# Optimization experiments

Measured on AMD Instinct MI355X. Metric: run time of the kernel, lower is better.

The kernel has to match this reference:

```python
import jax, jax.numpy as jnp
import numpy as np

TEMP = 0.1
DX = 64  # feature dim of x; W1 rows [0:DX] multiply x, rows [DX:] multiply y


def setup_inputs() -> dict:
    key = jax.random.key(0)
    k1, k2, k3, k4 = jax.random.split(key, 4)
    n, d, hidden = 1024, 64, 256
    x = jax.random.normal(k1, (n, d), dtype=jnp.float32)
    y = jax.random.normal(k2, (n, d), dtype=jnp.float32)
    W1 = jax.random.normal(k3, (2 * d, hidden), dtype=jnp.float32) * (1.0 / np.sqrt(2 * d))
    b1 = jnp.zeros((hidden,), dtype=jnp.float32)
    w2 = jax.random.normal(k4, (hidden,), dtype=jnp.float32) * (1.0 / np.sqrt(hidden))
    b2 = jnp.zeros((), dtype=jnp.float32)
    return {"x": x, "y": y, "W1": W1, "b1": b1, "w2": w2, "b2": b2}


def reference(x, y, W1, b1, w2, b2):
    n = y.shape[0]
    W1x, W1y = W1[:DX], W1[DX:]
    xp = x @ W1x                      # [n, hidden], indexed by j (x_tile[i,j] = x[j])
    yp = y @ W1y                      # [n, hidden], indexed by i (y_tile[i,j] = y[i])
    # Positive pairs: scorer(cat(x_i, y_i))
    pos = (jax.nn.relu(xp + yp + b1) @ w2 + b2) / TEMP          # [n]
    h = jax.nn.relu(yp[:, None, :] + xp[None, :, :] + b1)        # [n, n, hidden]
    scores = (h @ w2 + b2) / TEMP                                 # [n, n]
    lse = jax.nn.logsumexp(scores, axis=1)                        # [n]
    lower_bound = pos.mean() - (lse.mean() - jnp.log(jnp.float32(n)))
    return -lower_bound
```

## Files before the change

kernel.cpp:

```cpp
#include <hip/hip_runtime.h>
#include <math.h>

#define NN 1024
#define DD 64
#define HH 256
#define TEMP_INV 10.0f

typedef float v2f __attribute__((ext_vector_type(2)));


__global__ __launch_bounds__(256)
void k1_proj(const float* __restrict__ x, const float* __restrict__ y,
             const float* __restrict__ W1, const float* __restrict__ b1,
             float* __restrict__ x2T, float* __restrict__ y2)
{
    const int tid = threadIdx.x;
    const int i0 = blockIdx.x * 2;
    float ax0 = 0.f, ax1 = 0.f, ay0 = 0.f, ay1 = 0.f;
    #pragma unroll 8
    for (int kk = 0; kk < DD; ++kk) {
        const float wx = W1[kk * HH + tid];
        const float wy = W1[(DD + kk) * HH + tid];
        ax0 = fmaf(x[i0 * DD + kk],       wx, ax0);
        ax1 = fmaf(x[(i0 + 1) * DD + kk], wx, ax1);
        ay0 = fmaf(y[i0 * DD + kk],       wy, ay0);
        ay1 = fmaf(y[(i0 + 1) * DD + kk], wy, ay1);
    }
    const float b1t = b1[tid];
    *(float2*)&x2T[tid * NN + i0] = make_float2(ax0 + b1t, ax1 + b1t);
    y2[i0 * HH + tid]       = ay0;
    y2[(i0 + 1) * HH + tid] = ay1;
}

__global__ __launch_bounds__(256)
void k2_scores(const float* __restrict__ x2T, const float* __restrict__ y2,
               const float* __restrict__ w2, const float* __restrict__ b2,
               float* __restrict__ pmax, float* __restrict__ psum,
               float* __restrict__ pos)
{
    const int t  = threadIdx.x;
    const int bj = blockIdx.x;
    const int bi = blockIdx.y;
    const int j0 = bj * 64;
    const int rbase = bi * 32 + (t >> 5) * 4;
    const int cc = t & 31;

    const float* yb = y2 + (size_t)rbase * HH;
    const float* xb = x2T + j0 + cc * 2;

    v2f a0 = {0.f, 0.f}, a1 = {0.f, 0.f}, a2 = {0.f, 0.f}, a3 = {0.f, 0.f};
    const v2f zero = {0.f, 0.f};

    #pragma unroll 2
    for (int g = 0; g < HH / 4; ++g) {
        const int kb = g * 4;
        const float4 yr0 = *(const float4*)&yb[kb];
        const float4 yr1 = *(const float4*)&yb[HH + kb];
        const float4 yr2 = *(const float4*)&yb[2 * HH + kb];
        const float4 yr3 = *(const float4*)&yb[3 * HH + kb];
        const v2f xv0 = *(const v2f*)&xb[(size_t)(kb + 0) * NN];
        const v2f xv1 = *(const v2f*)&xb[(size_t)(kb + 1) * NN];
        const v2f xv2 = *(const v2f*)&xb[(size_t)(kb + 2) * NN];
        const v2f xv3 = *(const v2f*)&xb[(size_t)(kb + 3) * NN];
#define STEP(XV, Y0, Y1, Y2, Y3, WK)                                          \
        {                                                                     \
            const float wk = (WK);                                            \
            const v2f wv = {wk, wk};                                          \
            v2f z;                                                            \
            z = XV + (v2f){(Y0), (Y0)};                                       \
            z = __builtin_elementwise_max(z, zero);                           \
            a0 = z * wv + a0;                                                 \
            z = XV + (v2f){(Y1), (Y1)};                                       \
            z = __builtin_elementwise_max(z, zero);                           \
            a1 = z * wv + a1;                                                 \
            z = XV + (v2f){(Y2), (Y2)};                                       \
            z = __builtin_elementwise_max(z, zero);                           \
            a2 = z * wv + a2;                                                 \
            z = XV + (v2f){(Y3), (Y3)};                                       \
            z = __builtin_elementwise_max(z, zero);                           \
            a3 = z * wv + a3;                                                 \
        }
        STEP(xv0, yr0.x, yr1.x, yr2.x, yr3.x, w2[kb + 0])
        STEP(xv1, yr0.y, yr1.y, yr2.y, yr3.y, w2[kb + 1])
        STEP(xv2, yr0.z, yr1.z, yr2.z, yr3.z, w2[kb + 2])
        STEP(xv3, yr0.w, yr1.w, yr2.w, yr3.w, w2[kb + 3])
#undef STEP
    }

    const float bb = b2[0];
    const v2f bbv = {bb, bb};
    v2f sc[4];
    sc[0] = (a0 + bbv) * TEMP_INV;
    sc[1] = (a1 + bbv) * TEMP_INV;
    sc[2] = (a2 + bbv) * TEMP_INV;
    sc[3] = (a3 + bbv) * TEMP_INV;

    const int col0 = j0 + cc * 2;
    #pragma unroll
    for (int p = 0; p < 4; ++p) {
        const int row = rbase + p;
        if (row == col0)     pos[row] = sc[p].x;
        if (row == col0 + 1) pos[row] = sc[p].y;
    }

    float m[4], e[4];
    #pragma unroll
    for (int p = 0; p < 4; ++p) {
        m[p] = fmaxf(sc[p].x, sc[p].y);
        e[p] = __expf(sc[p].x - m[p]) + __expf(sc[p].y - m[p]);
    }
    #pragma unroll
    for (int mk = 16; mk >= 1; mk >>= 1) {
        #pragma unroll
        for (int p = 0; p < 4; ++p) {
            const float mo = __shfl_xor(m[p], mk);
            const float eo = __shfl_xor(e[p], mk);
            const float mn = fmaxf(m[p], mo);
            e[p] = e[p] * __expf(m[p] - mn) + eo * __expf(mo - mn);
            m[p] = mn;
        }
    }
    if (cc == 0) {
        #pragma unroll
        for (int p = 0; p < 4; ++p) {
            pmax[bj * NN + rbase + p] = m[p];
            psum[bj * NN + rbase + p] = e[p];
        }
    }
}

__global__ __launch_bounds__(1024)
void k3_final(const float* __restrict__ pmax, const float* __restrict__ psum,
              const float* __restrict__ pos, float* __restrict__ out)
{
    __shared__ float2 red[1024];
    const int tid = threadIdx.x;
    float M = pmax[tid], E = psum[tid];
    #pragma unroll
    for (int jc = 1; jc < 16; ++jc) {
        const float Mo = pmax[jc * NN + tid];
        const float Eo = psum[jc * NN + tid];
        const float Mn = fmaxf(M, Mo);
        E = E * __expf(M - Mn) + Eo * __expf(Mo - Mn);
        M = Mn;
    }
    red[tid] = make_float2(M + logf(E), pos[tid]);
    __syncthreads();
    for (int s = 512; s > 0; s >>= 1) {
        if (tid < s) {
            const float2 o = red[tid + s];
            float2 m2 = red[tid];
            m2.x += o.x; m2.y += o.y;
            red[tid] = m2;
        }
        __syncthreads();
    }
    if (tid == 0)
        out[0] = red[0].x / (float)NN - logf((float)NN) - red[0].y / (float)NN;
}

extern "C" void kernel_launch(void* const* d_in, const int* in_sizes, int n_in,
                              void* d_out, int out_size, void* d_ws, size_t ws_size,
                              hipStream_t stream)
{
    const float* x  = (const float*)d_in[0];
    const float* y  = (const float*)d_in[1];
    const float* W1 = (const float*)d_in[2];
    const float* b1 = (const float*)d_in[3];
    const float* w2 = (const float*)d_in[4];
    const float* b2 = (const float*)d_in[5];
    float* out = (float*)d_out;

    float* ws   = (float*)d_ws;
    float* x2T  = ws;
    float* y2   = x2T + HH * NN;
    float* pmax = y2 + NN * HH;
    float* psum = pmax + 16 * NN;
    float* pos  = psum + 16 * NN;

    hipLaunchKernelGGL(k1_proj, dim3(NN / 2), dim3(256), 0, stream,
                       x, y, W1, b1, x2T, y2);
    hipLaunchKernelGGL(k2_scores, dim3(16, 32), dim3(256), 0, stream,
                       x2T, y2, w2, b2, pmax, psum, pos);
    hipLaunchKernelGGL(k3_final, dim3(1), dim3(1024), 0, stream,
                       pmax, psum, pos, out);
}
```

Before: 47.10 us.

## Stage x2T tiles through LDS with register double-buffered prefetch in k2

The scores kernel now copies 64-row chunks of the transposed x projection into shared memory, cooperatively loading with float4, and prefetches the next chunk into registers while computing on the current one. y rows are also software-pipelined one step ahead in registers, and launch bounds request two blocks per CU. The aim is to replace strided per-thread global loads of x2T with coalesced loads and to hide their latency. The cost is extra syncthreads, LDS traffic and register pressure.

Measured after the change: 136.9 us. +190.7%, slower.

```diff
diff --git a/kernel.cpp b/kernel.cpp
--- a/kernel.cpp
+++ b/kernel.cpp
@@ -5,6 +5,8 @@
 #define DD 64
 #define HH 256
 #define TEMP_INV 10.0f
+#define KCH 64
+#define NCH 4
 
 typedef float v2f __attribute__((ext_vector_type(2)));
 
@@ -32,68 +34,85 @@
     y2[(i0 + 1) * HH + tid] = ay1;
 }
 
-__global__ __launch_bounds__(256)
+__global__ __launch_bounds__(256, 2)
 void k2_scores(const float* __restrict__ x2T, const float* __restrict__ y2,
                const float* __restrict__ w2, const float* __restrict__ b2,
                float* __restrict__ pmax, float* __restrict__ psum,
                float* __restrict__ pos)
 {
+    __shared__ float xs[KCH][64];
     const int t  = threadIdx.x;
     const int bj = blockIdx.x;
     const int bi = blockIdx.y;
     const int j0 = bj * 64;
-    const int rbase = bi * 32 + (t >> 5) * 4;
+    const int rr = t >> 5;
     const int cc = t & 31;
-
-    const float* yb = y2 + (size_t)rbase * HH;
-    const float* xb = x2T + j0 + cc * 2;
-
-    v2f a0 = {0.f, 0.f}, a1 = {0.f, 0.f}, a2 = {0.f, 0.f}, a3 = {0.f, 0.f};
+    const int rbase = bi * 32 + rr * 4;
+    const float* yb = y2 + rbase * HH;
+
+    const int sr  = t >> 4;
+    const int sc4 = (t & 15) * 4;
+
+    v2f acc[4];
+    #pragma unroll
+    for (int p = 0; p < 4; ++p) acc[p] = (v2f){0.f, 0.f};
     const v2f zero = {0.f, 0.f};
 
-    #pragma unroll 2
-    for (int g = 0; g < HH / 4; ++g) {
-        const int kb = g * 4;
-        const float4 yr0 = *(const float4*)&yb[kb];
-        const float4 yr1 = *(const float4*)&yb[HH + kb];
-        const float4 yr2 = *(const float4*)&yb[2 * HH + kb];
-        const float4 yr3 = *(const float4*)&yb[3 * HH + kb];
-        const v2f xv0 = *(const v2f*)&xb[(size_t)(kb + 0) * NN];
-        const v2f xv1 = *(const v2f*)&xb[(size_t)(kb + 1) * NN];
-        const v2f xv2 = *(const v2f*)&xb[(size_t)(kb + 2) * NN];
-        const v2f xv3 = *(const v2f*)&xb[(size_t)(kb + 3) * NN];
-#define STEP(XV, Y0, Y1, Y2, Y3, WK)                                          \
-        {                                                                     \
-            const float wk = (WK);                                            \
-            const v2f wv = {wk, wk};                                          \
-            v2f z;                                                            \
-            z = XV + (v2f){(Y0), (Y0)};                                       \
-            z = __builtin_elementwise_max(z, zero);                           \
-            a0 = z * wv + a0;                                                 \
-            z = XV + (v2f){(Y1), (Y1)};                                       \
-            z = __builtin_elementwise_max(z, zero);                           \
-            a1 = z * wv + a1;                                                 \
-            z = XV + (v2f){(Y2), (Y2)};                                       \
-            z = __builtin_elementwise_max(z, zero);                           \
-            a2 = z * wv + a2;                                                 \
-            z = XV + (v2f){(Y3), (Y3)};                                       \
-            z = __builtin_elementwise_max(z, zero);                           \
-            a3 = z * wv + a3;                                                 \
-        }
-        STEP(xv0, yr0.x, yr1.x, yr2.x, yr3.x, w2[kb + 0])
-        STEP(xv1, yr0.y, yr1.y, yr2.y, yr3.y, w2[kb + 1])
-        STEP(xv2, yr0.z, yr1.z, yr2.z, yr3.z, w2[kb + 2])
-        STEP(xv3, yr0.w, yr1.w, yr2.w, yr3.w, w2[kb + 3])
-#undef STEP
+    float4 sv[4];
+    #pragma unroll
+    for (int h = 0; h < 4; ++h)
+        sv[h] = *(const float4*)&x2T[(h * 16 + sr) * NN + j0 + sc4];
+
+    float4 yC[4], yN[4];
+    #pragma unroll
+    for (int p = 0; p < 4; ++p) yC[p] = *(const float4*)&yb[p * HH];
+
+    for (int c = 0; c < NCH; ++c) {
+        __syncthreads();
+        #pragma unroll
+        for (int h = 0; h < 4; ++h)
+            *(float4*)&xs[h * 16 + sr][sc4] = sv[h];
+        __syncthreads();
+        if (c + 1 < NCH) {
+            const int kn = (c + 1) * KCH;
+            #pragma unroll
+            for (int h = 0; h < 4; ++h)
+                sv[h] = *(const float4*)&x2T[(kn + h * 16 + sr) * NN + j0 + sc4];
+        }
+        #pragma unroll
+        for (int g = 0; g < 16; ++g) {
+            const int gg = c * 16 + g;
+            if (gg + 1 < 64) {
+                #pragma unroll
+                for (int p = 0; p < 4; ++p)
+                    yN[p] = *(const float4*)&yb[p * HH + (gg + 1) * 4];
+            }
+            #pragma unroll
+            for (int e = 0; e < 4; ++e) {
+                const int k  = gg * 4 + e;
+                const int kl = g * 4 + e;
+                const float wk = w2[k];
+                const v2f wv = {wk, wk};
+                const v2f xv = *(const v2f*)&xs[kl][cc * 2];
+                #pragma unroll
+                for (int p = 0; p < 4; ++p) {
+                    const float yv = (e == 0) ? yC[p].x : (e == 1) ? yC[p].y
+                                   : (e == 2) ? yC[p].z : yC[p].w;
+                    v2f z = xv + (v2f){yv, yv};
+                    z = __builtin_elementwise_max(z, zero);
+                    acc[p] = z * wv + acc[p];
+                }
+            }
+            #pragma unroll
+            for (int p = 0; p < 4; ++p) yC[p] = yN[p];
+        }
     }
 
     const float bb = b2[0];
     const v2f bbv = {bb, bb};
     v2f sc[4];
-    sc[0] = (a0 + bbv) * TEMP_INV;
-    sc[1] = (a1 + bbv) * TEMP_INV;
-    sc[2] = (a2 + bbv) * TEMP_INV;
-    sc[3] = (a3 + bbv) * TEMP_INV;
+    #pragma unroll
+    for (int p = 0; p < 4; ++p) sc[p] = (acc[p] + bbv) * TEMP_INV;
 
     const int col0 = j0 + cc * 2;
     #pragma unroll
```
